# Kernel tuning notes

Hardware: AMD Instinct MI355X
Metric: run time of the kernel (lower is better)

The kernel has to match this reference:

```python
import jax, jax.numpy as jnp
import numpy as np
from jax import lax

C3_TABLE = [(0, 1, 2), (1, 2, 3), (2, 3, 4), (3, 4, 5), (0, 4, 5), (0, 1, 5),
            (0, 1, 2, 3), (1, 2, 3, 4), (2, 3, 4, 5), (0, 3, 4, 5), (0, 1, 4, 5),
            (0, 1, 2, 5), (0, 1, 3, 4), (1, 2, 4, 5), (0, 2, 3, 5),
            (0, 1, 2, 3, 4, 5)]
TRIPLES = C3_TABLE[:6]   # 3-channel branches
QUADS   = C3_TABLE[6:15] # 4-channel branches
SEXTET  = C3_TABLE[15:]  # 6-channel branch
A = 1.7159
S = 2.0 / 3.0
DN = ('NCHW', 'OIHW', 'NCHW')


def _branch(x, idx, w, b):
    # x: [B,6,H,W]; gather channel subset, valid 5x5 conv to 1 output channel
    xg = x[:, jnp.array(idx), :, :]
    y = lax.conv_general_dilated(xg, w[None], (1, 1), 'VALID', dimension_numbers=DN)
    return y + b  # [B,1,H-4,W-4]


def setup_inputs() -> dict:
    key = jax.random.key(0)
    ks = jax.random.split(key, 7)
    B, H, W = 256, 142, 142
    return {
        'x':  jax.random.normal(ks[0], (B, 6, H, W), dtype=jnp.float32),
        'w3': jax.random.normal(ks[1], (6, 3, 5, 5), dtype=jnp.float32) * 0.1,
        'b3': jax.random.normal(ks[2], (6,), dtype=jnp.float32) * 0.1,
        'w4': jax.random.normal(ks[3], (9, 4, 5, 5), dtype=jnp.float32) * 0.1,
        'b4': jax.random.normal(ks[4], (9,), dtype=jnp.float32) * 0.1,
        'w6': jax.random.normal(ks[5], (1, 6, 5, 5), dtype=jnp.float32) * 0.1,
        'b6': jax.random.normal(ks[6], (1,), dtype=jnp.float32) * 0.1,
    }


def reference(x, w3, b3, w4, b4, w6, b6):
    outs = []
    for i, idx in enumerate(TRIPLES):
        outs.append(_branch(x, idx, w3[i], b3[i]))
    for i, idx in enumerate(QUADS):
        outs.append(_branch(x, idx, w4[i], b4[i]))
    outs.append(_branch(x, SEXTET[0], w6[0], b6[0]))
    y = jnp.concatenate(outs, axis=1)  # [B,16,H-4,W-4]
    return A * jnp.tanh(S * y)
```

## Files before the change

### kernel.cpp

```cpp
#include <hip/hip_runtime.h>
#include <hip/hip_bf16.h>


#define IH 142
#define IW 142
#define OH 138
#define OW 138
#define SROWS 16
#define PXP 148
#define ROW_H (PXP * 8)
#define ROW_D (PXP * 4)
#define NSLAB 12
#define NWG (NSLAB * 256)
#define CPX (NWG / 8)

typedef _Float16 f16x8 __attribute__((ext_vector_type(8)));
typedef float f32x4 __attribute__((ext_vector_type(4)));
typedef unsigned int u32x4 __attribute__((ext_vector_type(4)));

__device__ __constant__ const short WIDX16[16][6] = {
  {   0,    1,    2,   -1,   -1,   -1},
  {  -1,    3,    4,    5,   -1,   -1},
  {  -1,   -1,    6,    7,    8,   -1},
  {  -1,   -1,   -1,    9,   10,   11},
  {  12,   -1,   -1,   -1,   13,   14},
  {  15,   16,   -1,   -1,   -1,   17},
  {64+0, 64+1, 64+2, 64+3,   -1,   -1},
  {  -1, 64+4, 64+5, 64+6, 64+7,   -1},
  {  -1,   -1, 64+8, 64+9, 64+10, 64+11},
  {64+12,  -1,   -1, 64+13, 64+14, 64+15},
  {64+16, 64+17, -1,   -1, 64+18, 64+19},
  {64+20, 64+21, 64+22, -1,  -1, 64+23},
  {64+24, 64+25, -1, 64+26, 64+27,  -1},
  {  -1, 64+28, 64+29, -1, 64+30, 64+31},
  {64+32,  -1, 64+33, 64+34, -1, 64+35},
  {128+0, 128+1, 128+2, 128+3, 128+4, 128+5},
};

__global__ void wprep_kernel(const float* __restrict__ w3, const float* __restrict__ w4,
                             const float* __restrict__ w6, _Float16* __restrict__ tab) {
  int t = blockIdx.x * 256 + threadIdx.x;
  if (t >= 5120) return;
  int j = t & 7, lane = (t >> 3) & 63, dm = t >> 9;
  int dy = dm >> 1, m = dm & 1;
  int q = lane >> 4, oc = lane & 15;
  int k = m * 32 + q * 8 + j;
  int dx = k >> 3, c = k & 7;
  float v = 0.f;
  if (c < 6 && dx < 5) {
    int e = WIDX16[oc][c];
    if (e >= 0) {
      int src = e >> 6, blk = e & 63;
      const float* wp = (src == 0) ? w3 : (src == 1) ? w4 : w6;
      v = wp[blk * 25 + dy * 5 + dx];
    }
  }
  tab[t] = (_Float16)v;
}

__device__ __forceinline__ unsigned int pkh(float a, float b) {
  _Float16 ha = (_Float16)a, hb = (_Float16)b;
  unsigned short ua = __builtin_bit_cast(unsigned short, ha);
  unsigned short ub = __builtin_bit_cast(unsigned short, hb);
  return (unsigned int)ua | ((unsigned int)ub << 16);
}

__device__ __forceinline__ float act(float y) {
  const float TS = 1.9235933878519512f;
  const float e = __builtin_amdgcn_exp2f(y * TS);
  return fmaf(-2.f * 1.7159f, __builtin_amdgcn_rcpf(e + 1.f), 1.7159f);
}

__global__ __launch_bounds__(256, 4)
void c3_mfma(const float* __restrict__ x,
             const float* __restrict__ b3, const float* __restrict__ b4,
             const float* __restrict__ b6, const _Float16* __restrict__ tab,
             float* __restrict__ out) {
  __shared__ __attribute__((aligned(16))) _Float16 sh[SROWS * ROW_H];

  const int tid  = threadIdx.x;
  const int lane = tid & 63;
  const int w    = tid >> 6;

  const int hwid = (int)blockIdx.x + NSLAB * (int)blockIdx.z;
  const int swz  = (hwid & 7) * CPX + (hwid >> 3);
  const int sy   = swz % NSLAB;
  const int b    = swz / NSLAB;
  const int y0   = min(sy * 12, OH - 12);

  const int ocl = lane & 15;
  const int qq  = lane >> 4;

  const float* xb = x + (size_t)b * 6 * IH * IW;
  const size_t PLANE = (size_t)IH * IW;
  unsigned int* __restrict__ shu = (unsigned int*)sh;

  #pragma unroll 2
  for (int it = 0; it < 5; ++it) {
    const int idx = it * 256 + tid;
    if (idx < 1184) {
      const int row = idx / 74;
      const int px2 = idx - row * 74;
      u32x4 d0 = {0u, 0u, 0u, 0u}, d1 = {0u, 0u, 0u, 0u};
      if (px2 < 71) {
        const float* pr = xb + (size_t)(y0 + row) * IW + 2 * px2;
        const float2 v0 = *(const float2*)(pr);
        const float2 v1 = *(const float2*)(pr + PLANE);
        const float2 v2 = *(const float2*)(pr + 2 * PLANE);
        const float2 v3 = *(const float2*)(pr + 3 * PLANE);
        const float2 v4 = *(const float2*)(pr + 4 * PLANE);
        const float2 v5 = *(const float2*)(pr + 5 * PLANE);
        d0[0] = pkh(v0.x, v1.x); d0[1] = pkh(v2.x, v3.x); d0[2] = pkh(v4.x, v5.x);
        d1[0] = pkh(v0.y, v1.y); d1[1] = pkh(v2.y, v3.y); d1[2] = pkh(v4.y, v5.y);
      }
      *(u32x4*)&shu[row * ROW_D + px2 * 8]     = d0;
      *(u32x4*)&shu[row * ROW_D + px2 * 8 + 4] = d1;
    }
  }

  f16x8 Bf[5][2];
  #pragma unroll
  for (int dy = 0; dy < 5; ++dy)
    #pragma unroll
    for (int m = 0; m < 2; ++m)
      Bf[dy][m] = *(const f16x8*)(tab + ((size_t)((dy * 2 + m) * 64 + lane)) * 8);

  const float bv = (ocl < 6) ? b3[ocl] : (ocl < 15) ? b4[ocl - 6] : b6[0];

  __syncthreads();

  const size_t obase = ((size_t)b * 16 + ocl) * OH;
  #pragma unroll 1
  for (int i = 0; i < 14; ++i) {
    const int u = w + 4 * i;
    if (u >= 54) break;
    const int rp  = u / 9;
    const int t   = u - 9 * rp;
    const int x0t = min(t * 16, OW - 16);
    const int voff = (x0t + ocl + qq) * 8;

    f16x8 Wp[6][2];
    #pragma unroll
    for (int k = 0; k < 6; ++k) {
      Wp[k][0] = *(const f16x8*)&sh[(2 * rp + k) * ROW_H + voff];
      Wp[k][1] = *(const f16x8*)&sh[(2 * rp + k) * ROW_H + voff + 32];
    }

    f32x4 C0 = {bv, bv, bv, bv};
    f32x4 C1 = {bv, bv, bv, bv};
    __builtin_amdgcn_s_setprio(1);
    #pragma unroll
    for (int dy = 0; dy < 5; ++dy) {
      C0 = __builtin_amdgcn_mfma_f32_16x16x32_f16(Wp[dy][0],     Bf[dy][0], C0, 0, 0, 0);
      C1 = __builtin_amdgcn_mfma_f32_16x16x32_f16(Wp[dy + 1][0], Bf[dy][0], C1, 0, 0, 0);
      C0 = __builtin_amdgcn_mfma_f32_16x16x32_f16(Wp[dy][1],     Bf[dy][1], C0, 0, 0, 0);
      C1 = __builtin_amdgcn_mfma_f32_16x16x32_f16(Wp[dy + 1][1], Bf[dy][1], C1, 0, 0, 0);
    }
    __builtin_amdgcn_s_setprio(0);

    {
      float* p0 = out + (obase + (y0 + 2 * rp)) * OW + x0t + qq * 4;
      float* p1 = p0 + OW;
      *(float2*)p0       = make_float2(act(C0[0]), act(C0[1]));
      *(float2*)(p0 + 2) = make_float2(act(C0[2]), act(C0[3]));
      *(float2*)p1       = make_float2(act(C1[0]), act(C1[1]));
      *(float2*)(p1 + 2) = make_float2(act(C1[2]), act(C1[3]));
    }
  }
}

extern "C" void kernel_launch(void* const* d_in, const int* in_sizes, int n_in,
                              void* d_out, int out_size, void* d_ws, size_t ws_size,
                              hipStream_t stream) {
  const float* x  = (const float*)d_in[0];
  const float* w3 = (const float*)d_in[1];
  const float* b3 = (const float*)d_in[2];
  const float* w4 = (const float*)d_in[3];
  const float* b4 = (const float*)d_in[4];
  const float* w6 = (const float*)d_in[5];
  const float* b6 = (const float*)d_in[6];
  float* out = (float*)d_out;
  _Float16* tab = (_Float16*)d_ws;

  hipLaunchKernelGGL(wprep_kernel, dim3(20), dim3(256), 0, stream, w3, w4, w6, tab);

  dim3 grid(NSLAB, 1, 256);
  hipLaunchKernelGGL(c3_mfma, grid, dim3(256), 0, stream, x, b3, b4, b6, tab, out);
}
```

Before: 157.4 us.

## Split input staging in two and overlap the second half's loads with compute

The block now stages only the first 10 input rows into LDS before the first barrier. It then issues global loads for the remaining 6 rows into registers and computes the first half of the output row-pairs, which only need the staged rows. After that it converts and writes the held rows to LDS, synchronizes again and computes the second half. The aim is to hide global load latency behind MFMA work within each block, at the cost of one extra barrier and about 24 more live VGPRs, which could lower occupancy or cause spills under the 256x4 launch bound.

```diff
diff --git a/kernel.cpp b/kernel.cpp
--- a/kernel.cpp
+++ b/kernel.cpp
@@ -95,10 +95,10 @@
   const size_t PLANE = (size_t)IH * IW;
   unsigned int* __restrict__ shu = (unsigned int*)sh;
 
-  #pragma unroll 2
-  for (int it = 0; it < 5; ++it) {
+  #pragma unroll
+  for (int it = 0; it < 3; ++it) {
     const int idx = it * 256 + tid;
-    if (idx < 1184) {
+    if (idx < 740) {
       const int row = idx / 74;
       const int px2 = idx - row * 74;
       u32x4 d0 = {0u, 0u, 0u, 0u}, d1 = {0u, 0u, 0u, 0u};
@@ -129,10 +129,88 @@
 
   __syncthreads();
 
+  float2 hv[2][6];
+  #pragma unroll
+  for (int it = 0; it < 2; ++it) {
+    const int idx = it * 256 + tid;
+    if (idx < 444) {
+      const int row = 10 + idx / 74;
+      const int px2 = idx - (idx / 74) * 74;
+      if (px2 < 71) {
+        const float* pr = xb + (size_t)(y0 + row) * IW + 2 * px2;
+        hv[it][0] = *(const float2*)(pr);
+        hv[it][1] = *(const float2*)(pr + PLANE);
+        hv[it][2] = *(const float2*)(pr + 2 * PLANE);
+        hv[it][3] = *(const float2*)(pr + 3 * PLANE);
+        hv[it][4] = *(const float2*)(pr + 4 * PLANE);
+        hv[it][5] = *(const float2*)(pr + 5 * PLANE);
+      }
+    }
+  }
+
   const size_t obase = ((size_t)b * 16 + ocl) * OH;
+
   #pragma unroll 1
-  for (int i = 0; i < 14; ++i) {
+  for (int i = 0; i < 7; ++i) {
     const int u = w + 4 * i;
+    if (u >= 27) break;
+    const int rp  = u / 9;
+    const int t   = u - 9 * rp;
+    const int x0t = min(t * 16, OW - 16);
+    const int voff = (x0t + ocl + qq) * 8;
+
+    f16x8 Wp[6][2];
+    #pragma unroll
+    for (int k = 0; k < 6; ++k) {
+      Wp[k][0] = *(const f16x8*)&sh[(2 * rp + k) * ROW_H + voff];
+      Wp[k][1] = *(const f16x8*)&sh[(2 * rp + k) * ROW_H + voff + 32];
+    }
+
+    f32x4 C0 = {bv, bv, bv, bv};
+    f32x4 C1 = {bv, bv, bv, bv};
+    __builtin_amdgcn_s_setprio(1);
+    #pragma unroll
+    for (int dy = 0; dy < 5; ++dy) {
+      C0 = __builtin_amdgcn_mfma_f32_16x16x32_f16(Wp[dy][0],     Bf[dy][0], C0, 0, 0, 0);
+      C1 = __builtin_amdgcn_mfma_f32_16x16x32_f16(Wp[dy + 1][0], Bf[dy][0], C1, 0, 0, 0);
+      C0 = __builtin_amdgcn_mfma_f32_16x16x32_f16(Wp[dy][1],     Bf[dy][1], C0, 0, 0, 0);
+      C1 = __builtin_amdgcn_mfma_f32_16x16x32_f16(Wp[dy + 1][1], Bf[dy][1], C1, 0, 0, 0);
+    }
+    __builtin_amdgcn_s_setprio(0);
+
+    float* p0 = out + (obase + (y0 + 2 * rp)) * OW + x0t + qq * 4;
+    float* p1 = p0 + OW;
+    *(float2*)p0       = make_float2(act(C0[0]), act(C0[1]));
+    *(float2*)(p0 + 2) = make_float2(act(C0[2]), act(C0[3]));
+    *(float2*)p1       = make_float2(act(C1[0]), act(C1[1]));
+    *(float2*)(p1 + 2) = make_float2(act(C1[2]), act(C1[3]));
+  }
+
+  #pragma unroll
+  for (int it = 0; it < 2; ++it) {
+    const int idx = it * 256 + tid;
+    if (idx < 444) {
+      const int row = 10 + idx / 74;
+      const int px2 = idx - (idx / 74) * 74;
+      u32x4 d0 = {0u, 0u, 0u, 0u}, d1 = {0u, 0u, 0u, 0u};
+      if (px2 < 71) {
+        d0[0] = pkh(hv[it][0].x, hv[it][1].x);
+        d0[1] = pkh(hv[it][2].x, hv[it][3].x);
+        d0[2] = pkh(hv[it][4].x, hv[it][5].x);
+        d1[0] = pkh(hv[it][0].y, hv[it][1].y);
+        d1[1] = pkh(hv[it][2].y, hv[it][3].y);
+        d1[2] = pkh(hv[it][4].y, hv[it][5].y);
+      }
+      *(u32x4*)&shu[row * ROW_D + px2 * 8]     = d0;
+      *(u32x4*)&shu[row * ROW_D + px2 * 8 + 4] = d1;
+    }
+  }
+
+  __syncthreads();
+
+  #pragma unroll 1
+  for (int i = 0; i < 7; ++i) {
+    const int u = 27 + w + 4 * i;
     if (u >= 54) break;
     const int rp  = u / 9;
     const int t   = u - 9 * rp;
@@ -158,14 +236,12 @@
     }
     __builtin_amdgcn_s_setprio(0);
 
-    {
-      float* p0 = out + (obase + (y0 + 2 * rp)) * OW + x0t + qq * 4;
-      float* p1 = p0 + OW;
-      *(float2*)p0       = make_float2(act(C0[0]), act(C0[1]));
-      *(float2*)(p0 + 2) = make_float2(act(C0[2]), act(C0[3]));
-      *(float2*)p1       = make_float2(act(C1[0]), act(C1[1]));
-      *(float2*)(p1 + 2) = make_float2(act(C1[2]), act(C1[3]));
-    }
+    float* p0 = out + (obase + (y0 + 2 * rp)) * OW + x0t + qq * 4;
+    float* p1 = p0 + OW;
+    *(float2*)p0       = make_float2(act(C0[0]), act(C0[1]));
+    *(float2*)(p0 + 2) = make_float2(act(C0[2]), act(C0[3]));
+    *(float2*)p1       = make_float2(act(C1[0]), act(C1[1]));
+    *(float2*)(p1 + 2) = make_float2(act(C1[2]), act(C1[3]));
   }
 }
 
```

Result: no change. 160.2 us (+1.8%).
